# Kernel optimization log

Hardware: AMD Instinct MI355X
Metric: run time of the kernel (lower is better)

The kernel has to match this reference:

```python
import jax, jax.numpy as jnp
import numpy as np

SMOOTH = 1.0
MAX_DIST = 10


def _neighbor_conv(x):
    # 3x3 ones kernel with zero center, padding=1 (NCHW, C=1)
    k = jnp.ones((1, 1, 3, 3), x.dtype).at[0, 0, 1, 1].set(0.0)
    return jax.lax.conv_general_dilated(
        x, k, window_strides=(1, 1), padding=[(1, 1), (1, 1)],
        dimension_numbers=('NCHW', 'OIHW', 'NCHW'))


def _analyze_skeleton(skel):
    n = _neighbor_conv(skel)
    on = skel > 0.5
    endpoints = ((n == 1) & on).astype(skel.dtype)
    midpoints = ((n == 2) & on).astype(skel.dtype)
    junctions = ((n > 2) & on).astype(skel.dtype)
    return endpoints, midpoints, junctions


def _iou(p, g):
    inter = jnp.sum(p * g, axis=(2, 3))
    union = jnp.sum(p, axis=(2, 3)) + jnp.sum(g, axis=(2, 3)) - inter
    return (inter + SMOOTH) / (union + SMOOTH)


def _structural_similarity(pred_skel, gt_skel):
    pe, pm, pj = _analyze_skeleton(pred_skel)
    ge, gm, gj = _analyze_skeleton(gt_skel)
    e_iou, m_iou, j_iou = _iou(pe, ge), _iou(pm, gm), _iou(pj, gj)
    ge_c = jnp.sum(ge, axis=(2, 3))
    gj_c = jnp.sum(gj, axis=(2, 3))
    gm_c = jnp.sum(gm, axis=(2, 3))
    total = ge_c + gj_c + gm_c + SMOOTH
    loss = 1.0 - ((ge_c / total) * e_iou + (gj_c / total) * j_iou + (gm_c / total) * m_iou)
    return loss.mean()


def _maxpool3(x):
    return jax.lax.reduce_window(
        x, -jnp.inf, jax.lax.max,
        window_dimensions=(1, 1, 3, 3), window_strides=(1, 1, 1, 1),
        padding=[(0, 0), (0, 0), (1, 1), (1, 1)])


def _distance_approximation(target, reference):
    # Fixed MAX_DIST iterations; identical math to the torch early-exit loop
    # because new_points requires ~found_mask (no distance is overwritten).
    tgt_on = target > 0.5

    def step(carry, d):
        dilated, found, dist = carry
        dilated = _maxpool3(dilated)
        new = (dilated > 0.5) & tgt_on & (~found)
        dist = dist + d.astype(dist.dtype) * new.astype(dist.dtype)
        return (dilated, found | new, dist), None

    init = (reference, jnp.zeros(target.shape, bool), jnp.zeros_like(target))
    (_, found, dist), _ = jax.lax.scan(step, init, jnp.arange(1, MAX_DIST + 1, dtype=jnp.int32))
    unfound = tgt_on & (~found)
    dist = dist + jnp.asarray(MAX_DIST, dist.dtype) * unfound.astype(dist.dtype)
    total_points = jnp.sum(tgt_on.astype(dist.dtype), axis=(2, 3))
    return jnp.sum(dist, axis=(2, 3)) / (total_points + SMOOTH)


def _medial_axis_distance(pred_skel, gt_skel):
    p2g = _distance_approximation(pred_skel, gt_skel)
    g2p = _distance_approximation(gt_skel, pred_skel)
    return (((p2g + g2p) / 2.0) / MAX_DIST).mean()


def setup_inputs() -> dict:
    key = jax.random.key(0)
    k1, k2 = jax.random.split(key)
    B, C, H, W = 32, 1, 512, 512
    pred_skel = jax.random.uniform(k1, (B, C, H, W), dtype=jnp.float32)
    gt_skel = (jax.random.uniform(k2, (B, C, H, W), dtype=jnp.float32) < 0.1).astype(jnp.float32)
    return {"pred_skel": pred_skel, "gt_skel": gt_skel}


def reference(pred_skel, gt_skel):
    inter = jnp.sum(pred_skel * gt_skel, axis=(2, 3))
    psum = jnp.sum(pred_skel, axis=(2, 3))
    gsum = jnp.sum(gt_skel, axis=(2, 3))
    dice = (2.0 * inter + SMOOTH) / (psum + gsum + SMOOTH)
    dice_loss = 1.0 - dice.mean()
    structural_loss = _structural_similarity(pred_skel, gt_skel)
    medial_loss = _medial_axis_distance(pred_skel, gt_skel)
    avg_mag = (dice_loss + structural_loss + medial_loss) / 3.0
    bal_dice = dice_loss / (dice_loss + SMOOTH) * avg_mag
    bal_struct = structural_loss / (structural_loss + SMOOTH) * avg_mag
    bal_medial = medial_loss / (medial_loss + SMOOTH) * avg_mag
    return bal_dice + bal_struct + bal_medial
```

## Files before the change

### kernel.cpp

```cpp
#include <hip/hip_runtime.h>
#include <stdint.h>

#define BATCH 32
#define H 512
#define W 512
#define NACC 16
#define TH 32
#define HALO 9
#define RH (TH + 2*HALO)
#define NWORDS (RH*8)
#define NT 1024
#define NW (NT/64)
#define NTILE (H/TH)
#define NBLK (NTILE*BATCH)


__global__ __launch_bounds__(NT, 4) void fused_kernel(
    const float* __restrict__ pred, const float* __restrict__ gt,
    float* __restrict__ part)
{
    __shared__ uint64_t MpS[NWORDS + 2];
    __shared__ uint64_t MgS[NWORDS + 2];
    __shared__ uint64_t Ge[TH * 8];
    __shared__ uint64_t Gm[TH * 8];
    __shared__ uint64_t Gj[TH * 8];
    __shared__ float    EC[2][TH];
    __shared__ float    redf[NW][2];
    __shared__ unsigned redu[NW][5];

    uint64_t* Mp = MpS + 1;
    uint64_t* Mg = MgS + 1;

    int fid  = blockIdx.x;
    int b    = fid & 31;
    int tile = fid >> 5;

    const float* pimg = pred + (size_t)b * H * W;
    const float* gimg = gt   + (size_t)b * H * W;
    int y0 = tile * TH;
    int tid = threadIdx.x, lane = tid & 63, wid = tid >> 6;

    float v0 = 0.f, v1 = 0.f;
    for (int s0 = wid; s0 < NWORDS; s0 += 4 * NW) {
        float vp[4], vg[4];
        #pragma unroll
        for (int u = 0; u < 4; ++u) {
            int s = s0 + u * NW;
            vp[u] = 0.f; vg[u] = 0.f;
            int ry = y0 - HALO + (s >> 3);
            if (s < NWORDS && (unsigned)ry < (unsigned)H) {
                int i0 = ry * W + (s & 7) * 64 + lane;
                vp[u] = pimg[i0]; vg[u] = gimg[i0];
            }
        }
        #pragma unroll
        for (int u = 0; u < 4; ++u) {
            int s = s0 + u * NW;
            if (s < NWORDS) {
                unsigned long long mp = __ballot(vp[u] > 0.5f);
                unsigned long long mg = __ballot(vg[u] > 0.5f);
                if (lane == 0) { Mp[s] = mp; Mg[s] = mg; }
                int r = s >> 3;
                if (r >= HALO && r < HALO + TH) {
                    v1 += vp[u];
                    v0 += (vg[u] > 0.5f) ? vp[u] : 0.f;
                }
            }
        }
    }
    if (tid == 0) { MpS[0] = 0; MpS[NWORDS + 1] = 0; MgS[0] = 0; MgS[NWORDS + 1] = 0; }

    bool isStencil = tid >= 512;
    int idx = tid & 511;
    int qi = idx & 127, h2 = idx >> 7;
    int x4 = qi * 4;
    int ys = y0 + h2 * 8;
    float4 pm4 = make_float4(0, 0, 0, 0), pc4 = make_float4(0, 0, 0, 0);
    if (isStencil) {
        if (ys > 0) pm4 = *(const float4*)(pimg + (size_t)(ys - 1) * W + x4);
        pc4 = *(const float4*)(pimg + (size_t)ys * W + x4);
    }

    if (tid < 2 * TH) {
        int c = tid >> 5, r = tid & (TH - 1);
        int y = y0 + r, col = 255 + c;
        float sum = (y > 0     ? pimg[(size_t)(y - 1) * W + col] : 0.f)
                  +              pimg[(size_t)y * W + col]
                  + (y < H - 1 ? pimg[(size_t)(y + 1) * W + col] : 0.f);
        EC[c][r] = sum;
    }
    __syncthreads();

    uint64_t cpack = 0ULL;
    int dsum = 0, dcnt = 0;
    unsigned cge = 0, cgm = 0, cgj = 0;

    if (isStencil) {
        int wdx0 = (qi & 64) >> 4;
        if (lane < 32) {
            int ry = h2 * 8 + (lane >> 2);
            int w  = wdx0 + (lane & 3);
            int oM = (HALO + ry) * 8 + w;
            bool wl = (w > 0), wr = (w < 7);
            uint64_t A  = Mg[oM - 8], Bm = Mg[oM], Cm = Mg[oM + 8];
            uint64_t AL = wl ? Mg[oM - 9] : 0ULL, AR = wr ? Mg[oM - 7] : 0ULL;
            uint64_t BL = wl ? Mg[oM - 1] : 0ULL, BR = wr ? Mg[oM + 1] : 0ULL;
            uint64_t CL = wl ? Mg[oM + 7] : 0ULL, CR = wr ? Mg[oM + 9] : 0ULL;
            uint64_t Aw = (A  << 1) | (AL >> 63), Ae = (A  >> 1) | (AR << 63);
            uint64_t Bw = (Bm << 1) | (BL >> 63), Be = (Bm >> 1) | (BR << 63);
            uint64_t Cw = (Cm << 1) | (CL >> 63), Ce = (Cm >> 1) | (CR << 63);
            uint64_t c1, c2, c3, c5, t;
            t = Aw ^ A;  uint64_t s1 = t ^ Ae;  c1 = (Aw & A)  | (Ae & t);
            t = Bw ^ Be; uint64_t s2 = t ^ Cw;  c2 = (Bw & Be) | (Cw & t);
            t = Cm ^ Ce; uint64_t s3 = t ^ s1;  c3 = (Cm & Ce) | (s1 & t);
            uint64_t b0 = s2 ^ s3, c4 = s2 & s3;
            t = c1 ^ c2; uint64_t s5 = t ^ c3;  c5 = (c1 & c2) | (c3 & t);
            uint64_t b1 = s5 ^ c4, c6 = s5 & c4;
            uint64_t b2 = c5 ^ c6, b3 = c5 & c6;
            uint64_t nz23 = ~(b2 | b3);
            uint64_t ge = Bm & b0 & ~b1 & nz23;
            uint64_t gm = Bm & b1 & ~b0 & nz23;
            uint64_t gj = Bm & (b2 | b3 | (b1 & b0));
            Ge[ry * 8 + w] = ge; Gm[ry * 8 + w] = gm; Gj[ry * 8 + w] = gj;
            cge = (unsigned)__popcll(ge);
            cgm = (unsigned)__popcll(gm);
            cgj = (unsigned)__popcll(gj);
        }

        int wdx = qi >> 4;
        int ss = (qi & 15) * 4;

        for (int r = 0; r < 8; ++r) {
            int y = ys + r;
            float4 pp4 = (y < H - 1) ? *(const float4*)(pimg + (size_t)(y + 1) * W + x4)
                                     : make_float4(0, 0, 0, 0);
            int ry = h2 * 8 + r;
            uint64_t gew = Ge[ry * 8 + wdx];
            uint64_t gmw = Gm[ry * 8 + wdx];
            uint64_t gjw = Gj[ry * 8 + wdx];

            float ps[6];
            ps[1] = pm4.x + pc4.x + pp4.x; ps[2] = pm4.y + pc4.y + pp4.y;
            ps[3] = pm4.z + pc4.z + pp4.z; ps[4] = pm4.w + pc4.w + pp4.w;
            float psl = __shfl_up(ps[4], 1, 64);
            float psr = __shfl_down(ps[1], 1, 64);
            if (lane == 0)  psl = (qi == 0)   ? 0.f : EC[0][ry];
            if (lane == 63) psr = (qi == 127) ? 0.f : EC[1][ry];
            ps[0] = psl; ps[5] = psr;

            float pcv[4] = {pc4.x, pc4.y, pc4.z, pc4.w};
            #pragma unroll
            for (int j = 0; j < 4; ++j) {
                float np = ps[j] + ps[j + 1] + ps[j + 2] - pcv[j];
                bool pon = pcv[j] > 0.5f;
                bool pe  = pon && (np == 1.f);
                bool pmb = pon && (np == 2.f);
                bool pjb = pon && (np > 2.f);
                unsigned geb = (unsigned)(gew >> (ss + j)) & 1u;
                unsigned gmb = (unsigned)(gmw >> (ss + j)) & 1u;
                unsigned gjb = (unsigned)(gjw >> (ss + j)) & 1u;
                cpack += (uint64_t)pe
                       | ((uint64_t)pmb << 7)
                       | ((uint64_t)pjb << 14)
                       | ((uint64_t)(pe  && geb) << 21)
                       | ((uint64_t)(pmb && gmb) << 28)
                       | ((uint64_t)(pjb && gjb) << 35);
            }
            pm4 = pc4; pc4 = pp4;
        }
    } else {
        bool isP = tid < 256;
        int di = tid & 255;
        int o  = (HALO + (di >> 3)) * 8 + (di & 7);
        int w  = di & 7;
        bool wL = (w > 0), wR = (w < 7);
        const uint64_t* MT = isP ? Mp : Mg;
        const uint64_t* MV = isP ? Mg : Mp;

        uint64_t T = MT[o];
        dcnt = __popcll(T);
        dsum = dcnt;
        uint64_t VM = MV[o];
        uint64_t VL = wL ? MV[o - 1] : 0ULL;
        uint64_t VR = wR ? MV[o + 1] : 0ULL;
        uint64_t C = VM;

        #pragma unroll
        for (int a = 1; a <= 9; ++a) {
            int lo = o - 8 * a, hi = o + 8 * a;
            uint64_t NM = MV[lo] | MV[hi];
            uint64_t NL = wL ? (MV[lo - 1] | MV[hi - 1]) : 0ULL;
            uint64_t NR = wR ? (MV[lo + 1] | MV[hi + 1]) : 0ULL;
            uint64_t SL = NL, SM = NM, SR = NR;
            const int m = a - 1;
            if (m >= 1) {
                SM |= (SM << 1) | (SM >> 1) | (SL >> 63) | (SR << 63);
                SL |= SL << 1; SR |= SR >> 1;
            }
            if (m >= 2) {
                const int s = (m == 2) ? 1 : 2;
                SM |= (SM << s) | (SM >> s) | (SL >> (64 - s)) | (SR << (64 - s));
                SL |= SL << s; SR |= SR >> s;
            }
            if (m >= 4) {
                const int s = (m - 3 < 4) ? (m - 3) : 4;
                SM |= (SM << s) | (SM >> s) | (SL >> (64 - s)) | (SR << (64 - s));
                SL |= SL << s; SR |= SR >> s;
            }
            if (m >= 8) {
                const int s = m - 7;
                SM |= (SM << s) | (SM >> s) | (SL >> (64 - s)) | (SR << (64 - s));
                SL |= SL << s; SR |= SR >> s;
            }
            C |= SM;
            VL |= NL; VM |= NM; VR |= NR;
            C |= (VM << a) | (VM >> a) | (VL >> (64 - a)) | (VR << (64 - a));
            uint64_t rem = T & ~C;
            dsum += __popcll(rem);
            if (__all(rem == 0ULL)) break;
        }
    }

    unsigned r0, r1, r2, r3, r4;
    if (isStencil) {
        unsigned c_pe = (unsigned)( cpack        & 0x7F);
        unsigned c_pm = (unsigned)((cpack >> 7 ) & 0x7F);
        unsigned c_pj = (unsigned)((cpack >> 14) & 0x7F);
        unsigned c_ie = (unsigned)((cpack >> 21) & 0x7F);
        unsigned c_im = (unsigned)((cpack >> 28) & 0x7F);
        unsigned c_ij = (unsigned)((cpack >> 35) & 0x7F);
        r0 = c_pe | (c_pm << 16); r1 = c_pj | (c_ie << 16); r2 = c_im | (c_ij << 16);
        r3 = cge | (cgm << 16);   r4 = cgj;
    } else {
        r0 = (unsigned)dsum | ((unsigned)dcnt << 16);
        r1 = 0; r2 = 0; r3 = 0; r4 = 0;
    }
    #pragma unroll
    for (int off = 32; off; off >>= 1) {
        v0 += __shfl_down(v0, off, 64);
        v1 += __shfl_down(v1, off, 64);
        r0 += __shfl_down(r0, off, 64);
        r1 += __shfl_down(r1, off, 64);
        r2 += __shfl_down(r2, off, 64);
        r3 += __shfl_down(r3, off, 64);
        r4 += __shfl_down(r4, off, 64);
    }
    if (lane == 0) {
        redf[wid][0] = v0; redf[wid][1] = v1;
        redu[wid][0] = r0; redu[wid][1] = r1; redu[wid][2] = r2;
        redu[wid][3] = r3; redu[wid][4] = r4;
    }
    __syncthreads();
    if (tid < 16) {
        int k = tid;
        float s = 0.f;
        if (k < 2) {
            #pragma unroll
            for (int wv = 0; wv < NW; ++wv) s += redf[wv][k];
        } else {
            static const uint8_t WB[16] = {0,0, 4, 8,8,8, 8,8,8, 8,8,8, 0,0,4,4};
            static const uint8_t WC[16] = {0,0, 4, 8,8,8, 8,8,8, 8,8,8, 4,4,4,4};
            static const uint8_t RG[16] = {0,0, 0, 0,0,1, 3,3,4, 1,2,2, 0,0,0,0};
            static const uint8_t HI[16] = {0,0, 1, 0,1,0, 0,1,0, 1,0,1, 0,1,0,1};
            unsigned u = 0;
            for (int wv = WB[k]; wv < WB[k] + WC[k]; ++wv)
                u += (redu[wv][RG[k]] >> (HI[k] * 16)) & 0xFFFFu;
            s = (float)u;
        }
        part[fid * NACC + k] = s;
    }
}

__global__ __launch_bounds__(512) void final_kernel(
    const float* __restrict__ part, float* __restrict__ out)
{
    __shared__ float sacc[BATCH][NACC];
    __shared__ float tri[BATCH][3];
    int t = threadIdx.x;
    {
        int b = t >> 4, k = t & 15;
        float s = 0.f;
        #pragma unroll 4
        for (int j = 0; j < NTILE; ++j)
            s += part[((j << 5) + b) * NACC + k];
        sacc[b][k] = s;
    }
    __syncthreads();
    if (t < BATCH) {
        const float* a = sacc[t];
        float inter = a[0], psum = a[1], gsum = a[2];
        float dice = (2.f * inter + 1.f) / (psum + gsum + 1.f);

        float pe = a[3], pm = a[4], pj = a[5];
        float ge = a[6], gm = a[7], gj = a[8];
        float ie = a[9], im = a[10], ij = a[11];
        float e_iou = (ie + 1.f) / (pe + ge - ie + 1.f);
        float m_iou = (im + 1.f) / (pm + gm - im + 1.f);
        float j_iou = (ij + 1.f) / (pj + gj - ij + 1.f);
        float total = ge + gj + gm + 1.f;
        float sloss = 1.f - ((ge / total) * e_iou + (gj / total) * j_iou + (gm / total) * m_iou);

        float p2g = a[12] / (a[13] + 1.f);
        float g2p = a[14] / (a[15] + 1.f);
        float med = ((p2g + g2p) * 0.5f) / 10.f;
        tri[t][0] = dice; tri[t][1] = sloss; tri[t][2] = med;
    }
    __syncthreads();
    if (t == 0) {
        float dice = 0.f, sloss = 0.f, med = 0.f;
        for (int b = 0; b < BATCH; ++b) {
            dice += tri[b][0]; sloss += tri[b][1]; med += tri[b][2];
        }
        float dice_loss  = 1.f - dice / (float)BATCH;
        float structural = sloss / (float)BATCH;
        float medial     = med / (float)BATCH;
        float avg = (dice_loss + structural + medial) / 3.f;
        float r = dice_loss  / (dice_loss  + 1.f) * avg
                + structural / (structural + 1.f) * avg
                + medial     / (medial     + 1.f) * avg;
        out[0] = r;
    }
}

extern "C" void kernel_launch(void* const* d_in, const int* in_sizes, int n_in,
                              void* d_out, int out_size, void* d_ws, size_t ws_size,
                              hipStream_t stream)
{
    const float* pred = (const float*)d_in[0];
    const float* gt   = (const float*)d_in[1];
    float* part = (float*)d_ws;
    float* out  = (float*)d_out;

    fused_kernel<<<dim3(NBLK), NT, 0, stream>>>(pred, gt, part);
    final_kernel<<<1, 512, 0, stream>>>(part, out);
}
```

Baseline: 117.1 us.

## Split fused kernel into global bitmask pass plus separate stencil and distance blocks

The single fused kernel is split in two. A mask kernel reads each tile's own rows without halo, writes the pred and gt bitmasks to global workspace and accumulates the dice sums. A second kernel launches twice as many 512-thread blocks: half compute the skeleton stencil counts and half compute the distance dilation, each loading its bitmask window from global memory. This removes redundant halo reads of the float inputs and lets the stencil and distance work run on separate blocks in parallel. The cost is an extra launch and a global round trip for the masks.

```diff
diff --git a/kernel.cpp b/kernel.cpp
--- a/kernel.cpp
+++ b/kernel.cpp
@@ -8,104 +8,127 @@
 #define TH 32
 #define HALO 9
 #define RH (TH + 2*HALO)
-#define NWORDS (RH*8)
-#define NT 1024
-#define NW (NT/64)
+#define NT1 1024
+#define NW1 16
 #define NTILE (H/TH)
 #define NBLK (NTILE*BATCH)
 
 
-__global__ __launch_bounds__(NT, 4) void fused_kernel(
+#define MROW(bb, y) (((size_t)(bb) * H + (size_t)(y)) * 8)
+
+__global__ __launch_bounds__(NT1, 4) void mask_kernel(
     const float* __restrict__ pred, const float* __restrict__ gt,
-    float* __restrict__ part)
+    float* __restrict__ part, uint64_t* __restrict__ Mpg,
+    uint64_t* __restrict__ Mgg)
 {
-    __shared__ uint64_t MpS[NWORDS + 2];
-    __shared__ uint64_t MgS[NWORDS + 2];
-    __shared__ uint64_t Ge[TH * 8];
-    __shared__ uint64_t Gm[TH * 8];
-    __shared__ uint64_t Gj[TH * 8];
-    __shared__ float    EC[2][TH];
-    __shared__ float    redf[NW][2];
-    __shared__ unsigned redu[NW][5];
-
-    uint64_t* Mp = MpS + 1;
-    uint64_t* Mg = MgS + 1;
-
+    __shared__ float redf[NW1][2];
     int fid  = blockIdx.x;
     int b    = fid & 31;
     int tile = fid >> 5;
-
     const float* pimg = pred + (size_t)b * H * W;
     const float* gimg = gt   + (size_t)b * H * W;
     int y0 = tile * TH;
     int tid = threadIdx.x, lane = tid & 63, wid = tid >> 6;
 
     float v0 = 0.f, v1 = 0.f;
-    for (int s0 = wid; s0 < NWORDS; s0 += 4 * NW) {
+    int s = (wid < 8) ? wid + 80 : wid + 64;
+    #pragma unroll
+    for (int g = 0; g < 4; ++g) {
         float vp[4], vg[4];
         #pragma unroll
         for (int u = 0; u < 4; ++u) {
-            int s = s0 + u * NW;
-            vp[u] = 0.f; vg[u] = 0.f;
-            int ry = y0 - HALO + (s >> 3);
-            if (s < NWORDS && (unsigned)ry < (unsigned)H) {
-                int i0 = ry * W + (s & 7) * 64 + lane;
-                vp[u] = pimg[i0]; vg[u] = gimg[i0];
-            }
+            int ss = s + u * 16;
+            int ry = y0 - HALO + (ss >> 3);
+            int i0 = ry * W + (ss & 7) * 64 + lane;
+            vp[u] = pimg[i0]; vg[u] = gimg[i0];
         }
         #pragma unroll
         for (int u = 0; u < 4; ++u) {
-            int s = s0 + u * NW;
-            if (s < NWORDS) {
-                unsigned long long mp = __ballot(vp[u] > 0.5f);
-                unsigned long long mg = __ballot(vg[u] > 0.5f);
-                if (lane == 0) { Mp[s] = mp; Mg[s] = mg; }
-                int r = s >> 3;
-                if (r >= HALO && r < HALO + TH) {
-                    v1 += vp[u];
-                    v0 += (vg[u] > 0.5f) ? vp[u] : 0.f;
-                }
-            }
-        }
-    }
-    if (tid == 0) { MpS[0] = 0; MpS[NWORDS + 1] = 0; MgS[0] = 0; MgS[NWORDS + 1] = 0; }
-
-    bool isStencil = tid >= 512;
-    int idx = tid & 511;
-    int qi = idx & 127, h2 = idx >> 7;
-    int x4 = qi * 4;
-    int ys = y0 + h2 * 8;
-    float4 pm4 = make_float4(0, 0, 0, 0), pc4 = make_float4(0, 0, 0, 0);
+            int ss = s + u * 16;
+            unsigned long long mp = __ballot(vp[u] > 0.5f);
+            unsigned long long mg = __ballot(vg[u] > 0.5f);
+            int ry = y0 - HALO + (ss >> 3);
+            if (lane == 0) {
+                Mpg[MROW(b, ry) + (ss & 7)] = mp;
+                Mgg[MROW(b, ry) + (ss & 7)] = mg;
+            }
+            v1 += vp[u];
+            v0 += (vg[u] > 0.5f) ? vp[u] : 0.f;
+        }
+        s += 64;
+    }
+    #pragma unroll
+    for (int off = 32; off; off >>= 1) {
+        v0 += __shfl_down(v0, off, 64);
+        v1 += __shfl_down(v1, off, 64);
+    }
+    if (lane == 0) { redf[wid][0] = v0; redf[wid][1] = v1; }
+    __syncthreads();
+    if (tid < 2) {
+        float t = 0.f;
+        #pragma unroll
+        for (int wv = 0; wv < NW1; ++wv) t += redf[wv][tid];
+        part[fid * NACC + tid] = t;
+    }
+}
+
+__global__ __launch_bounds__(512, 4) void sd_kernel(
+    const float* __restrict__ pred, float* __restrict__ part,
+    const uint64_t* __restrict__ Mpg, const uint64_t* __restrict__ Mgg)
+{
+    __shared__ uint64_t Mg34[34 * 8];
+    __shared__ uint64_t Ge[TH * 8];
+    __shared__ uint64_t Gm[TH * 8];
+    __shared__ uint64_t Gj[TH * 8];
+    __shared__ uint64_t MpT[RH * 8];
+    __shared__ uint64_t MgT[RH * 8];
+    __shared__ float    EC[2][TH];
+    __shared__ unsigned redu[8][5];
+
+    int bid = blockIdx.x;
+    bool isStencil = bid < NBLK;
+    int fid  = isStencil ? bid : bid - NBLK;
+    int b    = fid & 31;
+    int tile = fid >> 5;
+    int y0 = tile * TH;
+    int tid = threadIdx.x, lane = tid & 63, wid = tid >> 6;
+
+    uint64_t cpack = 0ULL;
+    unsigned cge = 0, cgm = 0, cgj = 0;
+    int dsum = 0, dcnt = 0;
+
     if (isStencil) {
+        const float* pimg = pred + (size_t)b * H * W;
+        int qi = tid & 127, h2 = tid >> 7;
+        int x4 = qi * 4;
+        int ys = y0 + h2 * 8;
+        float4 pm4 = make_float4(0, 0, 0, 0), pc4;
         if (ys > 0) pm4 = *(const float4*)(pimg + (size_t)(ys - 1) * W + x4);
         pc4 = *(const float4*)(pimg + (size_t)ys * W + x4);
-    }
-
-    if (tid < 2 * TH) {
-        int c = tid >> 5, r = tid & (TH - 1);
-        int y = y0 + r, col = 255 + c;
-        float sum = (y > 0     ? pimg[(size_t)(y - 1) * W + col] : 0.f)
-                  +              pimg[(size_t)y * W + col]
-                  + (y < H - 1 ? pimg[(size_t)(y + 1) * W + col] : 0.f);
-        EC[c][r] = sum;
-    }
-    __syncthreads();
-
-    uint64_t cpack = 0ULL;
-    int dsum = 0, dcnt = 0;
-    unsigned cge = 0, cgm = 0, cgj = 0;
-
-    if (isStencil) {
-        int wdx0 = (qi & 64) >> 4;
-        if (lane < 32) {
-            int ry = h2 * 8 + (lane >> 2);
-            int w  = wdx0 + (lane & 3);
-            int oM = (HALO + ry) * 8 + w;
+
+        for (int i = tid; i < 34 * 8; i += 512) {
+            int y = y0 - 1 + (i >> 3);
+            Mg34[i] = ((unsigned)y < (unsigned)H) ? Mgg[MROW(b, y) + (i & 7)]
+                                                  : 0ULL;
+        }
+        if (tid < 2 * TH) {
+            int c = tid >> 5, r = tid & (TH - 1);
+            int y = y0 + r, col = 255 + c;
+            float sum = (y > 0     ? pimg[(size_t)(y - 1) * W + col] : 0.f)
+                      +              pimg[(size_t)y * W + col]
+                      + (y < H - 1 ? pimg[(size_t)(y + 1) * W + col] : 0.f);
+            EC[c][r] = sum;
+        }
+        __syncthreads();
+
+        if (tid < 256) {
+            int r = tid >> 3, w = tid & 7;
             bool wl = (w > 0), wr = (w < 7);
-            uint64_t A  = Mg[oM - 8], Bm = Mg[oM], Cm = Mg[oM + 8];
-            uint64_t AL = wl ? Mg[oM - 9] : 0ULL, AR = wr ? Mg[oM - 7] : 0ULL;
-            uint64_t BL = wl ? Mg[oM - 1] : 0ULL, BR = wr ? Mg[oM + 1] : 0ULL;
-            uint64_t CL = wl ? Mg[oM + 7] : 0ULL, CR = wr ? Mg[oM + 9] : 0ULL;
+            const uint64_t* base = Mg34 + r * 8 + w;
+            uint64_t A  = base[0],  Bm = base[8],  Cm = base[16];
+            uint64_t AL = wl ? base[-1] : 0ULL, AR = wr ? base[1]  : 0ULL;
+            uint64_t BL = wl ? base[7]  : 0ULL, BR = wr ? base[9]  : 0ULL;
+            uint64_t CL = wl ? base[15] : 0ULL, CR = wr ? base[17] : 0ULL;
             uint64_t Aw = (A  << 1) | (AL >> 63), Ae = (A  >> 1) | (AR << 63);
             uint64_t Bw = (Bm << 1) | (BL >> 63), Be = (Bm >> 1) | (BR << 63);
             uint64_t Cw = (Cm << 1) | (CL >> 63), Ce = (Cm >> 1) | (CR << 63);
@@ -121,15 +144,15 @@
             uint64_t ge = Bm & b0 & ~b1 & nz23;
             uint64_t gm = Bm & b1 & ~b0 & nz23;
             uint64_t gj = Bm & (b2 | b3 | (b1 & b0));
-            Ge[ry * 8 + w] = ge; Gm[ry * 8 + w] = gm; Gj[ry * 8 + w] = gj;
+            Ge[tid] = ge; Gm[tid] = gm; Gj[tid] = gj;
             cge = (unsigned)__popcll(ge);
             cgm = (unsigned)__popcll(gm);
             cgj = (unsigned)__popcll(gj);
         }
+        __syncthreads();
 
         int wdx = qi >> 4;
         int ss = (qi & 15) * 4;
-
         for (int r = 0; r < 8; ++r) {
             int y = ys + r;
             float4 pp4 = (y < H - 1) ? *(const float4*)(pimg + (size_t)(y + 1) * W + x4)
@@ -169,13 +192,24 @@
             pm4 = pc4; pc4 = pp4;
         }
     } else {
+        for (int i = tid; i < 2 * RH * 8; i += 512) {
+            int j = (i < RH * 8) ? i : i - RH * 8;
+            int y = y0 - HALO + (j >> 3);
+            uint64_t v = 0ULL;
+            if ((unsigned)y < (unsigned)H)
+                v = (i < RH * 8) ? Mpg[MROW(b, y) + (j & 7)]
+                                 : Mgg[MROW(b, y) + (j & 7)];
+            if (i < RH * 8) MpT[j] = v; else MgT[j] = v;
+        }
+        __syncthreads();
+
         bool isP = tid < 256;
         int di = tid & 255;
         int o  = (HALO + (di >> 3)) * 8 + (di & 7);
         int w  = di & 7;
         bool wL = (w > 0), wR = (w < 7);
-        const uint64_t* MT = isP ? Mp : Mg;
-        const uint64_t* MV = isP ? Mg : Mp;
+        const uint64_t* MT = isP ? MpT : MgT;
+        const uint64_t* MV = isP ? MgT : MpT;
 
         uint64_t T = MT[o];
         dcnt = __popcll(T);
@@ -237,8 +271,6 @@
     }
     #pragma unroll
     for (int off = 32; off; off >>= 1) {
-        v0 += __shfl_down(v0, off, 64);
-        v1 += __shfl_down(v1, off, 64);
         r0 += __shfl_down(r0, off, 64);
         r1 += __shfl_down(r1, off, 64);
         r2 += __shfl_down(r2, off, 64);
@@ -246,28 +278,32 @@
         r4 += __shfl_down(r4, off, 64);
     }
     if (lane == 0) {
-        redf[wid][0] = v0; redf[wid][1] = v1;
         redu[wid][0] = r0; redu[wid][1] = r1; redu[wid][2] = r2;
         redu[wid][3] = r3; redu[wid][4] = r4;
     }
     __syncthreads();
-    if (tid < 16) {
-        int k = tid;
-        float s = 0.f;
-        if (k < 2) {
-            #pragma unroll
-            for (int wv = 0; wv < NW; ++wv) s += redf[wv][k];
-        } else {
-            static const uint8_t WB[16] = {0,0, 4, 8,8,8, 8,8,8, 8,8,8, 0,0,4,4};
-            static const uint8_t WC[16] = {0,0, 4, 8,8,8, 8,8,8, 8,8,8, 4,4,4,4};
-            static const uint8_t RG[16] = {0,0, 0, 0,0,1, 3,3,4, 1,2,2, 0,0,0,0};
-            static const uint8_t HI[16] = {0,0, 1, 0,1,0, 0,1,0, 1,0,1, 0,1,0,1};
+
+    if (isStencil) {
+        if (tid < 9) {
+            static const uint8_t KK[9] = {3,4,5, 6,7,8, 9,10,11};
+            static const uint8_t RG[9] = {0,0,1, 3,3,4, 1,2,2};
+            static const uint8_t HI[9] = {0,1,0, 0,1,0, 1,0,1};
+            static const uint8_t WC[9] = {8,8,8, 4,4,4, 8,8,8};
             unsigned u = 0;
-            for (int wv = WB[k]; wv < WB[k] + WC[k]; ++wv)
-                u += (redu[wv][RG[k]] >> (HI[k] * 16)) & 0xFFFFu;
-            s = (float)u;
-        }
-        part[fid * NACC + k] = s;
+            for (int wv = 0; wv < WC[tid]; ++wv)
+                u += (redu[wv][RG[tid]] >> (HI[tid] * 16)) & 0xFFFFu;
+            part[fid * NACC + KK[tid]] = (float)u;
+        }
+    } else {
+        if (tid < 5) {
+            static const uint8_t KK[5] = {12,13,14,15,2};
+            static const uint8_t WB[5] = {0,0,4,4,4};
+            static const uint8_t HI[5] = {0,1,0,1,1};
+            unsigned u = 0;
+            for (int wv = WB[tid]; wv < WB[tid] + 4; ++wv)
+                u += (redu[wv][0] >> (HI[tid] * 16)) & 0xFFFFu;
+            part[fid * NACC + KK[tid]] = (float)u;
+        }
     }
 }
 
@@ -329,8 +365,11 @@
     const float* pred = (const float*)d_in[0];
     const float* gt   = (const float*)d_in[1];
     float* part = (float*)d_ws;
+    uint64_t* Mpg = (uint64_t*)((char*)d_ws + 65536);
+    uint64_t* Mgg = Mpg + (size_t)BATCH * H * 8;
     float* out  = (float*)d_out;
 
-    fused_kernel<<<dim3(NBLK), NT, 0, stream>>>(pred, gt, part);
+    mask_kernel<<<dim3(NBLK), NT1, 0, stream>>>(pred, gt, part, Mpg, Mgg);
+    sd_kernel<<<dim3(2 * NBLK), 512, 0, stream>>>(pred, part, Mpg, Mgg);
     final_kernel<<<1, 512, 0, stream>>>(part, out);
 }
```

After: 114.0 us. 1.03x faster.
